# Optimization experiments

Hardware: AMD Instinct MI355X
Metric: run time of the kernel (lower is better)

The kernel has to match this reference:

```python
import jax, jax.numpy as jnp
import numpy as np

NUM_HEADS = 16


def setup_inputs() -> dict:
    key = jax.random.key(0)
    ks = jax.random.split(key, 8)
    B, W, D = 128, 512, 2048
    s = 1.0 / np.sqrt(D)
    return {
        "x": jax.random.normal(ks[0], (B, D), jnp.float32),
        "buffer": jax.random.normal(ks[1], (B, W, D), jnp.float32),
        "Wq": jax.random.normal(ks[2], (D, D), jnp.float32) * s,
        "Wk": jax.random.normal(ks[3], (D, D), jnp.float32) * s,
        "Wv": jax.random.normal(ks[4], (D, D), jnp.float32) * s,
        "Wo": jax.random.normal(ks[5], (D, D), jnp.float32) * s,
        "Wg": jax.random.normal(ks[6], (D, 2 * D), jnp.float32) * (1.0 / np.sqrt(2 * D)),
        "bg": jnp.zeros((D,), jnp.float32),
    }


def reference(x, buffer, Wq, Wk, Wv, Wo, Wg, bg):
    B, D = x.shape
    H = NUM_HEADS
    Dh = D // H
    scale = Dh ** -0.5
    # steady-state ring buffer update: roll left, append x at last slot
    kv_seq = jnp.concatenate([buffer[:, 1:], x[:, None, :]], axis=1)  # [B, W, D]
    # projections (nn.Linear: y = x @ W.T)
    q = (x @ Wq.T).reshape(B, H, Dh)                      # [B, H, Dh]
    k = (kv_seq @ Wk.T).reshape(B, -1, H, Dh)             # [B, W, H, Dh]
    v = (kv_seq @ Wv.T).reshape(B, -1, H, Dh)
    # single-query attention over the window
    logits = jnp.einsum("bhd,bshd->bhs", q, k) * scale    # [B, H, W]
    attn = jax.nn.softmax(logits, axis=-1)
    out = jnp.einsum("bhs,bshd->bhd", attn, v).reshape(B, D)
    out = out @ Wo.T
    # gated residual
    g = jax.nn.sigmoid(jnp.concatenate([x, out], axis=-1) @ Wg.T + bg)
    return x + g * out
```

## Files before the change

kernel.cpp:

```cpp
#include <hip/hip_runtime.h>
#include <hip/hip_bf16.h>
#include <math.h>

#define B_   128
#define W_   512
#define D_   2048
#define H_   16
#define DH_  128

typedef __attribute__((ext_vector_type(4))) float f32x4;
typedef __attribute__((ext_vector_type(8))) short bf16x8;

typedef const __attribute__((address_space(1))) void* gvp;
typedef __attribute__((address_space(3))) void* lvp;

__device__ inline short f2bf(float f) {
  union { __hip_bfloat16 h; short s; } u;
  u.h = __float2bfloat16(f);
  return u.s;
}
__device__ inline float bf2f(unsigned short u) {
  return __uint_as_float(((unsigned)u) << 16);
}

#define LGKM_BARRIER() do {                                   \
    asm volatile("s_waitcnt lgkmcnt(0)" ::: "memory");        \
    __builtin_amdgcn_sched_barrier(0);                        \
    __builtin_amdgcn_s_barrier();                             \
    __builtin_amdgcn_sched_barrier(0);                        \
  } while (0)

template<bool BBF16>
__global__ __launch_bounds__(256) void gemm_mfma(
    const float* __restrict__ A, int a_rs, long a_hs,
    const float* __restrict__ A2, int a2_k,
    const void* __restrict__ Bv, int b_rs, long b_hs,
    float* __restrict__ C, int c_rs, long c_hs, long c_ks,
    int Kblk)
{
  __shared__ char sm[2][24576];

  const int t  = threadIdx.x;
  const int w  = t >> 6, l = t & 63, lo = l & 15, hi = l >> 4;
  const int wm = w >> 1, wn = w & 1;
  const int n0   = blockIdx.x * 64;
  const int head = blockIdx.y;
  const int ks   = blockIdx.z;
  const int kbeg = ks * Kblk;
  const int nit  = Kblk >> 6;

  const float* Ab;
  {
    const float* base = A;
    int koff = kbeg;
    if (A2 && kbeg >= a2_k) { base = A2; koff = kbeg - a2_k; }
    Ab = base + head * a_hs + koff;
  }
  const float*          Bf = (const float*)Bv          + (BBF16 ? 0 : head * b_hs + (long)n0 * b_rs + kbeg);
  const unsigned short* Bh = (const unsigned short*)Bv + (BBF16 ? head * b_hs + (long)n0 * b_rs + kbeg : 0);

  const int ar = t >> 2;
  const int ak = (t & 3) * 16;

  f32x4 acc[4][2] = {};

  auto load_tiles = [&](int it, float4* ar4, float4* br4) {
    const float* Ait = Ab + it * 64;
#pragma unroll
    for (int p = 0; p < 2; ++p) {
      const float* src = Ait + (long)(p * 64 + ar) * a_rs + ak;
#pragma unroll
      for (int qq = 0; qq < 4; ++qq) ar4[p * 4 + qq] = *(const float4*)(src + qq * 4);
    }
    if (BBF16) {
      const char* src = (const char*)(Bh + (long)ar * b_rs + it * 64 + ak);
      br4[0] = *(const float4*)(src);
      br4[1] = *(const float4*)(src + 16);
    } else {
      const float* src = Bf + (long)ar * b_rs + it * 64 + ak;
#pragma unroll
      for (int qq = 0; qq < 4; ++qq) br4[qq] = *(const float4*)(src + qq * 4);
    }
  };

  auto write_tiles = [&](int buf, const float4* ar4, const float4* br4) {
    char* As = sm[buf];
    char* Bs = sm[buf] + 16384;
#pragma unroll
    for (int p = 0; p < 2; ++p) {
      int m = p * 64 + ar;
      int base = m * 128 + ak * 2;
      int swz = (m & 7) << 4;
#pragma unroll
      for (int h2 = 0; h2 < 2; ++h2) {
        bf16x8 v;
        const float* f = (const float*)(ar4 + p * 4);
#pragma unroll
        for (int j = 0; j < 8; ++j) v[j] = f2bf(f[h2 * 8 + j]);
        *(bf16x8*)(As + ((base + h2 * 16) ^ swz)) = v;
      }
    }
    {
      int n = ar;
      int base = n * 128 + ak * 2;
      int swz = (n & 7) << 4;
      if (BBF16) {
#pragma unroll
        for (int h2 = 0; h2 < 2; ++h2)
          *(bf16x8*)(Bs + ((base + h2 * 16) ^ swz)) = ((const bf16x8*)br4)[h2];
      } else {
#pragma unroll
        for (int h2 = 0; h2 < 2; ++h2) {
          bf16x8 v;
          const float* f = (const float*)br4;
#pragma unroll
          for (int j = 0; j < 8; ++j) v[j] = f2bf(f[h2 * 8 + j]);
          *(bf16x8*)(Bs + ((base + h2 * 16) ^ swz)) = v;
        }
      }
    }
  };

  auto compute = [&](int buf) {
    const char* As = sm[buf];
    const char* Bs = sm[buf] + 16384;
#pragma unroll
    for (int kk = 0; kk < 2; ++kk) {
      bf16x8 af[4], bfr[2];
#pragma unroll
      for (int mi = 0; mi < 4; ++mi) {
        int m = wm * 64 + mi * 16 + lo;
        af[mi] = *(const bf16x8*)(As + ((m * 128 + (kk * 32 + hi * 8) * 2) ^ ((m & 7) << 4)));
      }
#pragma unroll
      for (int ni = 0; ni < 2; ++ni) {
        int n = wn * 32 + ni * 16 + lo;
        bfr[ni] = *(const bf16x8*)(Bs + ((n * 128 + (kk * 32 + hi * 8) * 2) ^ ((n & 7) << 4)));
      }
#pragma unroll
      for (int mi = 0; mi < 4; ++mi)
#pragma unroll
        for (int ni = 0; ni < 2; ++ni)
          acc[mi][ni] = __builtin_amdgcn_mfma_f32_16x16x32_bf16(af[mi], bfr[ni], acc[mi][ni], 0, 0, 0);
    }
  };

  float4 ar4[8], br4[4];
  load_tiles(0, ar4, br4);
  write_tiles(0, ar4, br4);
  __syncthreads();
  for (int it = 0; it < nit; ++it) {
    float4 na[8], nb[4];
    if (it + 1 < nit) load_tiles(it + 1, na, nb);
    compute(it & 1);
    if (it + 1 < nit) write_tiles((it + 1) & 1, na, nb);
    __syncthreads();
  }

  float* Cb = C + c_ks * ks + c_hs * head + n0;
#pragma unroll
  for (int mi = 0; mi < 4; ++mi)
#pragma unroll
    for (int ni = 0; ni < 2; ++ni)
#pragma unroll
      for (int r = 0; r < 4; ++r)
        Cb[(long)(wm * 64 + mi * 16 + hi * 4 + r) * c_rs + (wn * 32 + ni * 16 + lo)] = acc[mi][ni][r];
}

__global__ __launch_bounds__(256) void transpose_wk(
    const float* __restrict__ Wk, unsigned short* __restrict__ WkT)
{
  __shared__ float tile[64][68];
  const int t  = threadIdx.x;
  const int e0 = blockIdx.x * 64;
  const int d0 = blockIdx.y * 64;
  const int h  = blockIdx.z;
  {
    int d = t >> 2, eq = (t & 3) * 16;
    const float* src = Wk + (long)(h * DH_ + d0 + d) * D_ + e0 + eq;
#pragma unroll
    for (int qq = 0; qq < 4; ++qq)
      *(float4*)&tile[d][eq + qq * 4] = *(const float4*)(src + qq * 4);
  }
  __syncthreads();
  {
    int e = t >> 2, dq = (t & 3) * 16;
    unsigned short* dst = WkT + ((long)h * D_ + e0 + e) * DH_ + d0 + dq;
    bf16x8 v0, v1;
#pragma unroll
    for (int j = 0; j < 8; ++j) v0[j] = f2bf(tile[dq + j][e]);
#pragma unroll
    for (int j = 0; j < 8; ++j) v1[j] = f2bf(tile[dq + 8 + j][e]);
    *(bf16x8*)dst = v0;
    *(bf16x8*)(dst + 8) = v1;
  }
}

__global__ void reduce_add_k(const float* __restrict__ part, int ns, long stride,
                             long n, float* __restrict__ out)
{
  for (long i = (long)blockIdx.x * blockDim.x + threadIdx.x; i < n;
       i += (long)gridDim.x * blockDim.x) {
    float s = 0.f;
    for (int k = 0; k < ns; ++k) s += part[k * stride + i];
    out[i] = s;
  }
}

__global__ __launch_bounds__(1024, 4) void fused_attn(
    const float* __restrict__ x, const float* __restrict__ buffer,
    const float* __restrict__ qt, unsigned short* __restrict__ part,
    float* __restrict__ ml)
{
  __shared__ float kv[2 * 8 * 2048];
  __shared__ float lacc[16][8][16];
  __shared__ float pbuf[16][8];
  __shared__ float sbuf[16];

  const int b    = blockIdx.x;
  const int half = blockIdx.y;
  const int t    = threadIdx.x;
  const int w    = t >> 6;
  const int lane = t & 63;
  const int lo   = lane & 15;
  const int hi   = lane >> 4;
  const char* kvb = (const char*)kv;

  bf16x8 afrag[4];
  {
    const float* qrow = qt + ((long)b * H_ + lo) * D_;
    const float sc = 0.088388347648318447f;
#pragma unroll
    for (int kk = 0; kk < 4; ++kk) {
      int e0 = w * 128 + kk * 32 + hi * 8;
#pragma unroll
      for (int j = 0; j < 8; ++j) afrag[kk][j] = f2bf(qrow[e0 + j] * sc);
    }
  }

  float accE[16][2];
#pragma unroll
  for (int h = 0; h < 16; ++h) { accE[h][0] = 0.f; accE[h][1] = 0.f; }
  float m_run = -1e30f, l_run = 0.f;

  auto stage = [&](int sb, int tl) {
#pragma unroll
    for (int r = 0; r < 4; ++r) {
      int s = r * 2 + (w >> 3);
      int inrow = (w & 7) * 1024 + lane * 16;
      int srco = inrow ^ (s << 4);
      int s_glob = half * 256 + tl * 8 + s;
      const float* row = (s_glob < W_ - 1)
          ? buffer + (((long)(b * W_ + s_glob + 1)) << 11)
          : x + ((long)b << 11);
      __builtin_amdgcn_global_load_lds(
          (gvp)(row + (srco >> 2)),
          (lvp)(kv + sb * 16384 + r * 4096 + w * 256), 16, 0, 0);
    }
  };

  stage(0, 0);
  __syncthreads();

  for (int tile = 0; tile < 32; ++tile) {
    const int buf  = tile & 1;
    const int bufo = buf * 65536;

    if (tile + 1 < 32) stage(buf ^ 1, tile + 1);

    {
      f32x4 c4 = {0.f, 0.f, 0.f, 0.f};
      const int srow = lo & 7;
#pragma unroll
      for (int kk = 0; kk < 4; ++kk) {
        unsigned B0 = (unsigned)(srow * 8192 + (w * 128 + kk * 32 + hi * 8) * 4);
        unsigned o1 = B0 ^ (unsigned)(srow << 4);
        float4 f1 = *(const float4*)(kvb + bufo + o1);
        float4 f2 = *(const float4*)(kvb + bufo + (o1 ^ 16u));
        unsigned u[4];
        u[0] = __builtin_amdgcn_perm(__float_as_uint(f1.y), __float_as_uint(f1.x), 0x07060302u);
        u[1] = __builtin_amdgcn_perm(__float_as_uint(f1.w), __float_as_uint(f1.z), 0x07060302u);
        u[2] = __builtin_amdgcn_perm(__float_as_uint(f2.y), __float_as_uint(f2.x), 0x07060302u);
        u[3] = __builtin_amdgcn_perm(__float_as_uint(f2.w), __float_as_uint(f2.z), 0x07060302u);
        bf16x8 bf;
        __builtin_memcpy(&bf, u, 16);
        c4 = __builtin_amdgcn_mfma_f32_16x16x32_bf16(afrag[kk], bf, c4, 0, 0, 0);
      }
      if (lo < 8) *(f32x4*)&lacc[w][lo][hi * 4] = c4;
    }
    LGKM_BARRIER();

    if (w < 4) {
      const int h = w * 4 + hi;
      const int s = lo & 7;
      float v = 0.f;
#pragma unroll
      for (int ww = 0; ww < 16; ++ww) v += lacc[ww][s][h];
      float mt = v;
      mt = fmaxf(mt, __shfl_xor(mt, 1));
      mt = fmaxf(mt, __shfl_xor(mt, 2));
      mt = fmaxf(mt, __shfl_xor(mt, 4));
      float m_new = fmaxf(m_run, mt);
      float scl = __expf(m_run - m_new);
      float p = __expf(v - m_new);
      float ps = p;
      ps += __shfl_xor(ps, 1);
      ps += __shfl_xor(ps, 2);
      ps += __shfl_xor(ps, 4);
      l_run = l_run * scl + ps;
      m_run = m_new;
      if (lo < 8) pbuf[h][s] = p;
      if (lo == 0) sbuf[h] = scl;
    }
    LGKM_BARRIER();

    const unsigned ebyte = (unsigned)((w * 128 + lane * 2) * 4);
    float2 kvp[8];
#pragma unroll
    for (int s = 0; s < 8; ++s) {
      unsigned Bx = (unsigned)(s * 8192) + ebyte;
      kvp[s] = *(const float2*)(kvb + bufo + (Bx ^ (unsigned)(s << 4)));
    }
#pragma unroll
    for (int h = 0; h < 16; ++h) {
      float scl = sbuf[h];
      float a0 = accE[h][0] * scl, a1 = accE[h][1] * scl;
      float4 pA = *(const float4*)&pbuf[h][0];
      float4 pB = *(const float4*)&pbuf[h][4];
      a0 += pA.x * kvp[0].x + pA.y * kvp[1].x + pA.z * kvp[2].x + pA.w * kvp[3].x
          + pB.x * kvp[4].x + pB.y * kvp[5].x + pB.z * kvp[6].x + pB.w * kvp[7].x;
      a1 += pA.x * kvp[0].y + pA.y * kvp[1].y + pA.z * kvp[2].y + pA.w * kvp[3].y
          + pB.x * kvp[4].y + pB.y * kvp[5].y + pB.z * kvp[6].y + pB.w * kvp[7].y;
      accE[h][0] = a0; accE[h][1] = a1;
    }
    __syncthreads();
  }

  {
    long base = ((long)half * B_ + b) * H_;
#pragma unroll
    for (int h = 0; h < 16; ++h) {
      long idx = (base + h) * D_ + w * 128 + lane * 2;
      unsigned u0 = (unsigned short)f2bf(accE[h][0]);
      unsigned u1 = (unsigned short)f2bf(accE[h][1]);
      *(unsigned*)(part + idx) = u0 | (u1 << 16);
    }
    if (w < 4 && lo == 0) {
      ml[(base + w * 4 + hi) * 2 + 0] = m_run;
      ml[(base + w * 4 + hi) * 2 + 1] = l_run;
    }
  }
}

__global__ __launch_bounds__(256) void combine_k(
    const unsigned short* __restrict__ part, const float* __restrict__ ml,
    float* __restrict__ vt)
{
  const int bh = blockIdx.x;
  const float m0 = ml[bh * 2],          l0 = ml[bh * 2 + 1];
  const float m1 = ml[(2048 + bh) * 2], l1 = ml[(2048 + bh) * 2 + 1];
  const float M  = fmaxf(m0, m1);
  const float w0 = __expf(m0 - M), w1 = __expf(m1 - M);
  const float inv = 1.0f / (w0 * l0 + w1 * l1);
  const unsigned short* p0 = part + (long)bh * D_;
  const unsigned short* p1 = part + (long)(2048 + bh) * D_;
  float* out = vt + (long)bh * D_;

  const int e = threadIdx.x * 8;
  ushort4 a1 = *(const ushort4*)(p0 + e);
  ushort4 a2 = *(const ushort4*)(p0 + e + 4);
  ushort4 b1 = *(const ushort4*)(p1 + e);
  ushort4 b2 = *(const ushort4*)(p1 + e + 4);
  float oa[8], ob[8];
  oa[0]=bf2f(a1.x); oa[1]=bf2f(a1.y); oa[2]=bf2f(a1.z); oa[3]=bf2f(a1.w);
  oa[4]=bf2f(a2.x); oa[5]=bf2f(a2.y); oa[6]=bf2f(a2.z); oa[7]=bf2f(a2.w);
  ob[0]=bf2f(b1.x); ob[1]=bf2f(b1.y); ob[2]=bf2f(b1.z); ob[3]=bf2f(b1.w);
  ob[4]=bf2f(b2.x); ob[5]=bf2f(b2.y); ob[6]=bf2f(b2.z); ob[7]=bf2f(b2.w);
#pragma unroll
  for (int j = 0; j < 8; ++j) out[e + j] = (w0 * oa[j] + w1 * ob[j]) * inv;
}

__global__ __launch_bounds__(256) void gate_final_k(
    const float* __restrict__ part, const float* __restrict__ bg,
    const float* __restrict__ x, const float* __restrict__ out1,
    float* __restrict__ y)
{
  const long i = (long)blockIdx.x * 256 + threadIdx.x;
  float z = bg[i & (D_ - 1)];
#pragma unroll
  for (int k = 0; k < 8; ++k) z += part[(long)k * (B_ * D_) + i];
  const float g = 1.0f / (1.0f + expf(-z));
  y[i] = x[i] + g * out1[i];
}

extern "C" void kernel_launch(void* const* d_in, const int* in_sizes, int n_in,
                              void* d_out, int out_size, void* d_ws, size_t ws_size,
                              hipStream_t stream)
{
  const float* x      = (const float*)d_in[0];
  const float* buffer = (const float*)d_in[1];
  const float* Wq     = (const float*)d_in[2];
  const float* Wk     = (const float*)d_in[3];
  const float* Wv     = (const float*)d_in[4];
  const float* Wo     = (const float*)d_in[5];
  const float* Wg     = (const float*)d_in[6];
  const float* bg     = (const float*)d_in[7];
  float* y = (float*)d_out;

  float* ws    = (float*)d_ws;
  float* q     = ws;
  float* qt    = ws + 262144;
  float* vt    = qt;
  unsigned short* part_a = (unsigned short*)(ws + 4456448);
  float* ml    = ws + 8650752;
  float* o0    = ws + 8658944;
  float* o1    = ws + 8921088;
  float* partg = ws + 9183232;
  unsigned short* wkT = (unsigned short*)(ws + 11280384);

  const long S = (long)B_ * D_;

  transpose_wk<<<dim3(32, 2, 16), 256, 0, stream>>>(Wk, wkT);

  gemm_mfma<false><<<dim3(32, 1, 8), 256, 0, stream>>>(
      x, D_, 0, nullptr, 1 << 30, Wq, D_, 0, partg, D_, 0, S, 256);
  reduce_add_k<<<512, 256, 0, stream>>>(partg, 8, S, S, q);

  gemm_mfma<true><<<dim3(32, 16, 1), 256, 0, stream>>>(
      q, D_, DH_, nullptr, 1 << 30, wkT, DH_, (long)D_ * DH_,
      qt, H_ * D_, D_, 0, DH_);

  fused_attn<<<dim3(B_, 2), 1024, 0, stream>>>(x, buffer, qt, part_a, ml);
  combine_k<<<B_ * H_, 256, 0, stream>>>(part_a, ml, vt);

  gemm_mfma<false><<<dim3(2, 16, 8), 256, 0, stream>>>(
      vt, H_ * D_, D_, nullptr, 1 << 30, Wv, D_, (long)DH_ * D_,
      partg, D_, DH_, S, 256);
  reduce_add_k<<<512, 256, 0, stream>>>(partg, 8, S, S, o0);

  gemm_mfma<false><<<dim3(32, 1, 8), 256, 0, stream>>>(
      o0, D_, 0, nullptr, 1 << 30, Wo, D_, 0, partg, D_, 0, S, 256);
  reduce_add_k<<<512, 256, 0, stream>>>(partg, 8, S, S, o1);

  gemm_mfma<false><<<dim3(32, 1, 8), 256, 0, stream>>>(
      x, D_, 0, o1, D_, Wg, 2 * D_, 0, partg, D_, 0, S, 512);
  gate_final_k<<<1024, 256, 0, stream>>>(partg, bg, x, o1, y);

  (void)in_sizes; (void)n_in; (void)out_size; (void)ws_size;
}
```

Baseline: 252.2 us.

## Fuse split-softmax combine into Wv GEMM A-load and spread softmax over all waves

Removes the combine_k kernel and instead merges the two half-window bf16 partials with their (m,l) weights inside the Wv GEMM's A-tile load, so the fp32 combined vt tensor is never written to and re-read from global memory. In fused_attn, the softmax reduction is now spread across all 16 waves, one head per wave, with shuffle reductions instead of 4 waves doing serial 16-way sums. The lacc shared array is padded to [16][9][20], likely to reduce LDS bank conflicts. The V-row loads from LDS are hoisted before the barrier to overlap with the reduction. The trade-off is that the GEMM recomputes the combine weights per row per K-tile and reads both partial buffers, which adds ALU and global load work to its inner loop.

```diff
diff --git a/kernel.cpp b/kernel.cpp
--- a/kernel.cpp
+++ b/kernel.cpp
@@ -30,7 +30,7 @@
     __builtin_amdgcn_sched_barrier(0);                        \
   } while (0)
 
-template<bool BBF16>
+template<bool BBF16, int AMODE>
 __global__ __launch_bounds__(256) void gemm_mfma(
     const float* __restrict__ A, int a_rs, long a_hs,
     const float* __restrict__ A2, int a2_k,
@@ -49,8 +49,8 @@
   const int kbeg = ks * Kblk;
   const int nit  = Kblk >> 6;
 
-  const float* Ab;
-  {
+  const float* Ab = nullptr;
+  if (AMODE == 0) {
     const float* base = A;
     int koff = kbeg;
     if (A2 && kbeg >= a2_k) { base = A2; koff = kbeg - a2_k; }
@@ -65,12 +65,42 @@
   f32x4 acc[4][2] = {};
 
   auto load_tiles = [&](int it, float4* ar4, float4* br4) {
-    const float* Ait = Ab + it * 64;
-#pragma unroll
-    for (int p = 0; p < 2; ++p) {
-      const float* src = Ait + (long)(p * 64 + ar) * a_rs + ak;
-#pragma unroll
-      for (int qq = 0; qq < 4; ++qq) ar4[p * 4 + qq] = *(const float4*)(src + qq * 4);
+    if (AMODE == 0) {
+      const float* Ait = Ab + it * 64;
+#pragma unroll
+      for (int p = 0; p < 2; ++p) {
+        const float* src = Ait + (long)(p * 64 + ar) * a_rs + ak;
+#pragma unroll
+        for (int qq = 0; qq < 4; ++qq) ar4[p * 4 + qq] = *(const float4*)(src + qq * 4);
+      }
+    } else {
+      const unsigned short* pa = (const unsigned short*)A;
+      const float* mlp = A2;
+      const int col = kbeg + it * 64 + ak;
+#pragma unroll
+      for (int p = 0; p < 2; ++p) {
+        int m  = p * 64 + ar;
+        int bh = m * 16 + head;
+        float m0 = mlp[bh * 2],              l0 = mlp[bh * 2 + 1];
+        float m1 = mlp[(2048 + bh) * 2],     l1 = mlp[(2048 + bh) * 2 + 1];
+        float M  = fmaxf(m0, m1);
+        float w0 = __expf(m0 - M), w1 = __expf(m1 - M);
+        float inv = 1.0f / (w0 * l0 + w1 * l1);
+        w0 *= inv; w1 *= inv;
+        const unsigned short* r0 = pa + (long)bh * D_ + col;
+        const unsigned short* r1 = r0 + (long)B_ * H_ * D_;
+#pragma unroll
+        for (int q2 = 0; q2 < 2; ++q2) {
+          bf16x8 a0 = *(const bf16x8*)(r0 + q2 * 8);
+          bf16x8 a1 = *(const bf16x8*)(r1 + q2 * 8);
+          float out[8];
+#pragma unroll
+          for (int j = 0; j < 8; ++j)
+            out[j] = w0 * bf2f((unsigned short)a0[j]) + w1 * bf2f((unsigned short)a1[j]);
+          ar4[p * 4 + q2 * 2]     = make_float4(out[0], out[1], out[2], out[3]);
+          ar4[p * 4 + q2 * 2 + 1] = make_float4(out[4], out[5], out[6], out[7]);
+        }
+      }
     }
     if (BBF16) {
       const char* src = (const char*)(Bh + (long)ar * b_rs + it * 64 + ak);
@@ -213,7 +243,7 @@
     float* __restrict__ ml)
 {
   __shared__ float kv[2 * 8 * 2048];
-  __shared__ float lacc[16][8][16];
+  __shared__ float lacc[16][9][20];
   __shared__ float pbuf[16][8];
   __shared__ float sbuf[16];
 
@@ -288,14 +318,25 @@
       }
       if (lo < 8) *(f32x4*)&lacc[w][lo][hi * 4] = c4;
     }
+
+    float2 kvp[8];
+    {
+      const unsigned ebyte = (unsigned)((w * 128 + lane * 2) * 4);
+#pragma unroll
+      for (int s = 0; s < 8; ++s) {
+        unsigned Bx = (unsigned)(s * 8192) + ebyte;
+        kvp[s] = *(const float2*)(kvb + bufo + (Bx ^ (unsigned)(s << 4)));
+      }
+    }
     LGKM_BARRIER();
 
-    if (w < 4) {
-      const int h = w * 4 + hi;
-      const int s = lo & 7;
-      float v = 0.f;
-#pragma unroll
-      for (int ww = 0; ww < 16; ++ww) v += lacc[ww][s][h];
+    {
+      const int s   = lane & 7;
+      const int wwg = lane >> 3;
+      float v = lacc[wwg][s][w] + lacc[wwg + 8][s][w];
+      v += __shfl_xor(v, 8);
+      v += __shfl_xor(v, 16);
+      v += __shfl_xor(v, 32);
       float mt = v;
       mt = fmaxf(mt, __shfl_xor(mt, 1));
       mt = fmaxf(mt, __shfl_xor(mt, 2));
@@ -309,18 +350,11 @@
       ps += __shfl_xor(ps, 4);
       l_run = l_run * scl + ps;
       m_run = m_new;
-      if (lo < 8) pbuf[h][s] = p;
-      if (lo == 0) sbuf[h] = scl;
+      if (lane < 8) pbuf[w][lane] = p;
+      if (lane == 0) sbuf[w] = scl;
     }
     LGKM_BARRIER();
 
-    const unsigned ebyte = (unsigned)((w * 128 + lane * 2) * 4);
-    float2 kvp[8];
-#pragma unroll
-    for (int s = 0; s < 8; ++s) {
-      unsigned Bx = (unsigned)(s * 8192) + ebyte;
-      kvp[s] = *(const float2*)(kvb + bufo + (Bx ^ (unsigned)(s << 4)));
-    }
 #pragma unroll
     for (int h = 0; h < 16; ++h) {
       float scl = sbuf[h];
@@ -345,39 +379,11 @@
       unsigned u1 = (unsigned short)f2bf(accE[h][1]);
       *(unsigned*)(part + idx) = u0 | (u1 << 16);
     }
-    if (w < 4 && lo == 0) {
-      ml[(base + w * 4 + hi) * 2 + 0] = m_run;
-      ml[(base + w * 4 + hi) * 2 + 1] = l_run;
-    }
-  }
-}
-
-__global__ __launch_bounds__(256) void combine_k(
-    const unsigned short* __restrict__ part, const float* __restrict__ ml,
-    float* __restrict__ vt)
-{
-  const int bh = blockIdx.x;
-  const float m0 = ml[bh * 2],          l0 = ml[bh * 2 + 1];
-  const float m1 = ml[(2048 + bh) * 2], l1 = ml[(2048 + bh) * 2 + 1];
-  const float M  = fmaxf(m0, m1);
-  const float w0 = __expf(m0 - M), w1 = __expf(m1 - M);
-  const float inv = 1.0f / (w0 * l0 + w1 * l1);
-  const unsigned short* p0 = part + (long)bh * D_;
-  const unsigned short* p1 = part + (long)(2048 + bh) * D_;
-  float* out = vt + (long)bh * D_;
-
-  const int e = threadIdx.x * 8;
-  ushort4 a1 = *(const ushort4*)(p0 + e);
-  ushort4 a2 = *(const ushort4*)(p0 + e + 4);
-  ushort4 b1 = *(const ushort4*)(p1 + e);
-  ushort4 b2 = *(const ushort4*)(p1 + e + 4);
-  float oa[8], ob[8];
-  oa[0]=bf2f(a1.x); oa[1]=bf2f(a1.y); oa[2]=bf2f(a1.z); oa[3]=bf2f(a1.w);
-  oa[4]=bf2f(a2.x); oa[5]=bf2f(a2.y); oa[6]=bf2f(a2.z); oa[7]=bf2f(a2.w);
-  ob[0]=bf2f(b1.x); ob[1]=bf2f(b1.y); ob[2]=bf2f(b1.z); ob[3]=bf2f(b1.w);
-  ob[4]=bf2f(b2.x); ob[5]=bf2f(b2.y); ob[6]=bf2f(b2.z); ob[7]=bf2f(b2.w);
-#pragma unroll
-  for (int j = 0; j < 8; ++j) out[e + j] = (w0 * oa[j] + w1 * ob[j]) * inv;
+    if (lane == 0) {
+      ml[(base + w) * 2 + 0] = m_run;
+      ml[(base + w) * 2 + 1] = l_run;
+    }
+  }
 }
 
 __global__ __launch_bounds__(256) void gate_final_k(
@@ -410,7 +416,6 @@
   float* ws    = (float*)d_ws;
   float* q     = ws;
   float* qt    = ws + 262144;
-  float* vt    = qt;
   unsigned short* part_a = (unsigned short*)(ws + 4456448);
   float* ml    = ws + 8650752;
   float* o0    = ws + 8658944;
@@ -422,27 +427,26 @@
 
   transpose_wk<<<dim3(32, 2, 16), 256, 0, stream>>>(Wk, wkT);
 
-  gemm_mfma<false><<<dim3(32, 1, 8), 256, 0, stream>>>(
+  gemm_mfma<false, 0><<<dim3(32, 1, 8), 256, 0, stream>>>(
       x, D_, 0, nullptr, 1 << 30, Wq, D_, 0, partg, D_, 0, S, 256);
   reduce_add_k<<<512, 256, 0, stream>>>(partg, 8, S, S, q);
 
-  gemm_mfma<true><<<dim3(32, 16, 1), 256, 0, stream>>>(
+  gemm_mfma<true, 0><<<dim3(32, 16, 1), 256, 0, stream>>>(
       q, D_, DH_, nullptr, 1 << 30, wkT, DH_, (long)D_ * DH_,
       qt, H_ * D_, D_, 0, DH_);
 
   fused_attn<<<dim3(B_, 2), 1024, 0, stream>>>(x, buffer, qt, part_a, ml);
-  combine_k<<<B_ * H_, 256, 0, stream>>>(part_a, ml, vt);
-
-  gemm_mfma<false><<<dim3(2, 16, 8), 256, 0, stream>>>(
-      vt, H_ * D_, D_, nullptr, 1 << 30, Wv, D_, (long)DH_ * D_,
+
+  gemm_mfma<false, 1><<<dim3(2, 16, 8), 256, 0, stream>>>(
+      (const float*)part_a, 0, 0, ml, 0, Wv, D_, (long)DH_ * D_,
       partg, D_, DH_, S, 256);
   reduce_add_k<<<512, 256, 0, stream>>>(partg, 8, S, S, o0);
 
-  gemm_mfma<false><<<dim3(32, 1, 8), 256, 0, stream>>>(
+  gemm_mfma<false, 0><<<dim3(32, 1, 8), 256, 0, stream>>>(
       o0, D_, 0, nullptr, 1 << 30, Wo, D_, 0, partg, D_, 0, S, 256);
   reduce_add_k<<<512, 256, 0, stream>>>(partg, 8, S, S, o1);
 
-  gemm_mfma<false><<<dim3(32, 1, 8), 256, 0, stream>>>(
+  gemm_mfma<false, 0><<<dim3(32, 1, 8), 256, 0, stream>>>(
       x, D_, 0, o1, D_, Wg, 2 * D_, 0, partg, D_, 0, S, 512);
   gate_final_k<<<1024, 256, 0, stream>>>(partg, bg, x, o1, y);
 
```

Measured after the change: 244.8 us. 3.0% less time.
